# Kernel optimization log

Measured on AMD Instinct MI355X. Metric: run time of the kernel, lower is better.

The kernel has to match this reference:

```python
import jax, jax.numpy as jnp
import numpy as np

NQ = 14            # qubits = ceil(log2(16384))
DIM = 2 ** NQ
OUT = 1000         # out_features (slice last OUT probs)


def _apply_ry(state, theta, axis):
    """Apply RY(theta) on the qubit at `axis` of state shaped (B, 2,...,2).
    RY = [[cos(t/2), -sin(t/2)], [sin(t/2), cos(t/2)]] (real)."""
    c = jnp.cos(theta / 2)
    s = jnp.sin(theta / 2)
    x = jnp.moveaxis(state, axis, -1)
    x0, x1 = x[..., 0], x[..., 1]
    y = jnp.stack([c * x0 - s * x1, s * x0 + c * x1], axis=-1)
    return jnp.moveaxis(y, -1, axis)


def _apply_cz(state, axis):
    """CZ on adjacent qubits (axis, axis+1): flip sign of |11> amplitudes."""
    sign = jnp.ones((2, 2), state.dtype).at[1, 1].set(-1.0)
    shape = [1] * state.ndim
    shape[axis] = 2
    shape[axis + 1] = 2
    return state * sign.reshape(shape)


def _circuit(inp, weights, bias):
    B, F = inp.shape
    # AmplitudeEmbedding(pad_with=1, normalize=True)
    if F < DIM:
        inp = jnp.pad(inp, ((0, 0), (0, DIM - F)), constant_values=1.0)
    norm = jnp.sqrt(jnp.sum(inp * inp, axis=1, keepdims=True))
    state = (inp / norm).reshape((B,) + (2,) * NQ)
    # SimplifiedTwoDesign: initial RY layer (bias)
    for w in range(NQ):
        state = _apply_ry(state, bias[w], 1 + w)
    # entangling layers: even CZ/RY block then odd CZ/RY block
    nlayer = weights.shape[0]
    for l in range(nlayer):
        for start in (0, 1):
            for i in range(start, NQ - 1, 2):
                state = _apply_cz(state, 1 + i)
                state = _apply_ry(state, weights[l, i, 0], 1 + i)
                state = _apply_ry(state, weights[l, i, 1], 1 + i + 1)
    amps = state.reshape(B, DIM)
    probs = amps * amps  # real statevector -> |amp|^2
    return probs[:, -OUT:]


def setup_inputs() -> dict:
    key = jax.random.key(0)
    k1, k2, k3 = jax.random.split(key, 3)
    return {
        "input": jax.random.normal(k1, (512, 16384), dtype=jnp.float32),
        "weights": jax.random.normal(k2, (2, NQ - 1, 2), dtype=jnp.float32),
        "bias": jax.random.normal(k3, (NQ,), dtype=jnp.float32),
    }


def reference(input, weights, bias):
    return _circuit(input, weights, bias)
```

## Files before the change

### kernel.cpp

```cpp
#include <hip/hip_runtime.h>

#define NQ 14
#define DIM 16384
#define OUT_N 1000
#define PRUNED 2048

using v2f = __attribute__((ext_vector_type(2))) float;

__host__ __device__ constexpr int WI(int l, int i, int k) {
    return 14 + (l * 13 + i) * 2 + k;
}

__global__ void cs_kernel(const float* __restrict__ w,
                          const float* __restrict__ b,
                          float2* __restrict__ cs) {
    int g = threadIdx.x;
    if (g < 66) {
        float th = (g < NQ) ? b[g] : w[g - NQ];
        cs[g] = make_float2(cosf(0.5f * th), sinf(0.5f * th));
    }
}

__device__ __forceinline__ int swz(int a) { return a ^ ((a >> 5) & 31); }

template<int B, int NP>
__device__ __forceinline__ void ry(v2f* x, float c, float s) {
    if constexpr (B == 0) {
#pragma unroll
        for (int p = 0; p < NP; ++p) {
            float a0 = x[p].x, a1 = x[p].y;
            x[p].x = c * a0 - s * a1;
            x[p].y = s * a0 + c * a1;
        }
    } else {
        constexpr int pb = B - 1;
#pragma unroll
        for (int m = 0; m < NP / 2; ++m) {
            int p0 = ((m >> pb) << (pb + 1)) | (m & ((1 << pb) - 1));
            int p1 = p0 | (1 << pb);
            v2f lo = x[p0], hi = x[p1];
            x[p0] = lo * c - hi * s;
            x[p1] = hi * c + lo * s;
        }
    }
}

template<int BH, int BL, int NP>
__device__ __forceinline__ void cz(v2f* x) {
    static_assert(BH > BL, "");
    if constexpr (BL >= 1) {
#pragma unroll
        for (int p = 0; p < NP; ++p)
            if (((p >> (BH - 1)) & 1) && ((p >> (BL - 1)) & 1)) x[p] = -x[p];
    } else {
#pragma unroll
        for (int p = 0; p < NP; ++p)
            if ((p >> (BH - 1)) & 1) x[p].y = -x[p].y;
    }
}

#define BLK(BH, I0, I1, NP)                                       \
    cz<BH, BH - 1, NP>(x);                                        \
    { float2 cc = csv[I0]; ry<BH, NP>(x, cc.x, cc.y); }           \
    { float2 cd = csv[I1]; ry<BH - 1, NP>(x, cd.x, cd.y); }

__global__ __launch_bounds__(256, 2)
void qnnA(const float* __restrict__ in, const float2* __restrict__ csv,
          float* __restrict__ ws) {
    __shared__ float red[4];
    const int t = threadIdx.x;
    const int b = blockIdx.x;
    const float* __restrict__ xin = in + (size_t)b * DIM;

    v2f x[32];
#pragma unroll
    for (int p = 0; p < 32; ++p) {
        x[p].x = xin[((2 * p) << 8) | t];
        x[p].y = xin[((2 * p + 1) << 8) | t];
    }

    float pp = 0.f;
#pragma unroll
    for (int p = 0; p < 32; ++p) pp = fmaf(x[p].x, x[p].x, fmaf(x[p].y, x[p].y, pp));
#pragma unroll
    for (int d = 32; d; d >>= 1) pp += __shfl_xor(pp, d);
    if ((t & 63) == 0) red[t >> 6] = pp;
    __syncthreads();
    const float scale = 1.0f / sqrtf(red[0] + red[1] + red[2] + red[3]);

    { float2 cc;
      cc = csv[0]; ry<5, 32>(x, cc.x, cc.y);
      cc = csv[1]; ry<4, 32>(x, cc.x, cc.y);
      cc = csv[2]; ry<3, 32>(x, cc.x, cc.y);
      cc = csv[3]; ry<2, 32>(x, cc.x, cc.y);
      cc = csv[4]; ry<1, 32>(x, cc.x, cc.y);
      cc = csv[5]; ry<0, 32>(x, cc.x, cc.y); }
    BLK(5, WI(0,0,0), WI(0,0,1), 32)
    BLK(3, WI(0,2,0), WI(0,2,1), 32)
    BLK(1, WI(0,4,0), WI(0,4,1), 32)
    BLK(4, WI(0,1,0), WI(0,1,1), 32)
    BLK(2, WI(0,3,0), WI(0,3,1), 32)
    BLK(5, WI(1,0,0), WI(1,0,1), 32)
    BLK(3, WI(1,2,0), WI(1,2,1), 32)
    BLK(4, WI(1,1,0), WI(1,1,1), 32)

    float* __restrict__ wrow = ws + (size_t)b * PRUNED;
#pragma unroll
    for (int p = 28; p < 32; ++p) {
        wrow[((2 * p - 56) << 8) | t] = x[p].x * scale;
        wrow[((2 * p - 55) << 8) | t] = x[p].y * scale;
    }
}

__global__ __launch_bounds__(64, 4)
void qnnB(const float* __restrict__ ws, const float2* __restrict__ csv,
          float* __restrict__ out) {
    __shared__ float lds[PRUNED];
    const int s = threadIdx.x;
    const int r = blockIdx.x;

    v2f x[16];
    { const float4* __restrict__ src4 =
          (const float4*)(ws + (size_t)r * PRUNED + s * 32);
#pragma unroll
      for (int i = 0; i < 8; ++i) {
          float4 f = src4[i];
          x[2 * i].x = f.x; x[2 * i].y = f.y;
          x[2 * i + 1].x = f.z; x[2 * i + 1].y = f.w;
      } }

    { float2 cc;
      cc = csv[9];  ry<4, 16>(x, cc.x, cc.y);
      cc = csv[10]; ry<3, 16>(x, cc.x, cc.y);
      cc = csv[11]; ry<2, 16>(x, cc.x, cc.y);
      cc = csv[12]; ry<1, 16>(x, cc.x, cc.y);
      cc = csv[13]; ry<0, 16>(x, cc.x, cc.y); }
    BLK(3, WI(0,10,0), WI(0,10,1), 16)
    BLK(1, WI(0,12,0), WI(0,12,1), 16)
    BLK(2, WI(0,11,0), WI(0,11,1), 16)
    BLK(1, WI(1,12,0), WI(1,12,1), 16)

#pragma unroll
    for (int l = 0; l < 32; ++l)
        lds[swz((s << 5) | l)] = (l & 1) ? x[l >> 1].y : x[l >> 1].x;
    __syncthreads();
#pragma unroll
    for (int l = 0; l < 32; ++l) {
        float v = lds[swz(((s >> 4) << 9) | (l << 4) | (s & 15))];
        if (l & 1) x[l >> 1].y = v; else x[l >> 1].x = v;
    }

    { float2 cc;
      cc = csv[6]; ry<3, 16>(x, cc.x, cc.y);
      cc = csv[7]; ry<2, 16>(x, cc.x, cc.y);
      cc = csv[8]; ry<1, 16>(x, cc.x, cc.y); }
    BLK(3, WI(0,6,0), WI(0,6,1), 16)
    BLK(1, WI(0,8,0), WI(0,8,1), 16)
    BLK(4, WI(0,5,0), WI(0,5,1), 16)
    BLK(2, WI(0,7,0), WI(0,7,1), 16)
    BLK(3, WI(1,6,0), WI(1,6,1), 16)

#pragma unroll
    for (int l = 0; l < 32; ++l)
        lds[swz(((s >> 4) << 9) | (l << 4) | (s & 15))] =
            (l & 1) ? x[l >> 1].y : x[l >> 1].x;
    __syncthreads();
#pragma unroll
    for (int l = 0; l < 32; ++l) {
        float v = lds[swz(((s >> 2) << 7) | (l << 2) | (s & 3))];
        if (l & 1) x[l >> 1].y = v; else x[l >> 1].x = v;
    }

    BLK(2, WI(0,9,0),  WI(0,9,1),  16)
    BLK(3, WI(1,8,0),  WI(1,8,1),  16)
    BLK(1, WI(1,10,0), WI(1,10,1), 16)
    BLK(4, WI(1,7,0),  WI(1,7,1),  16)
    BLK(2, WI(1,9,0),  WI(1,9,1),  16)

#pragma unroll
    for (int l = 0; l < 32; ++l)
        lds[swz(((s >> 2) << 7) | (l << 2) | (s & 3))] =
            (l & 1) ? x[l >> 1].y : x[l >> 1].x;
    __syncthreads();
#pragma unroll
    for (int l = 0; l < 32; ++l) {
        float v = lds[swz((l << 6) | s)];
        if (l & 1) x[l >> 1].y = v; else x[l >> 1].x = v;
    }

    BLK(3, WI(1,4,0), WI(1,4,1), 16)
    BLK(4, WI(1,3,0), WI(1,3,1), 16)
    BLK(2, WI(1,5,0), WI(1,5,1), 16)

#pragma unroll
    for (int l = 0; l < 32; ++l)
        lds[swz((l << 6) | s)] = (l & 1) ? x[l >> 1].y : x[l >> 1].x;
    __syncthreads();
#pragma unroll
    for (int l = 0; l < 32; ++l) {
        float v = lds[swz((s << 5) | l)];
        if (l & 1) x[l >> 1].y = v; else x[l >> 1].x = v;
    }

    BLK(2, WI(1,11,0), WI(1,11,1), 16)

    if (s >= 32) {
        float* __restrict__ orow = out + (size_t)r * OUT_N;
        const int base = s * 32 - 1048;
#pragma unroll
        for (int l = 0; l < 32; ++l) {
            int j = base + l;
            float v = (l & 1) ? x[l >> 1].y : x[l >> 1].x;
            if (j >= 0) orow[j] = v * v;
        }
    }
}

extern "C" void kernel_launch(void* const* d_in, const int* in_sizes, int n_in,
                              void* d_out, int out_size, void* d_ws, size_t ws_size,
                              hipStream_t stream) {
    const float* in   = (const float*)d_in[0];
    const float* wts  = (const float*)d_in[1];
    const float* bias = (const float*)d_in[2];
    float* out = (float*)d_out;

    float2* cs  = (float2*)d_ws;
    float*  buf = (float*)d_ws + 1024;

    const int nb = in_sizes[0] / DIM;

    cs_kernel<<<1, 128, 0, stream>>>(wts, bias, cs);
    qnnA<<<nb, 256, 0, stream>>>(in, (const float2*)cs, buf);
    qnnB<<<nb, 64, 0, stream>>>(buf, (const float2*)cs, out);
}
```

Baseline: 92.06 us.

## Fuse three launches into one kernel with LDS transposes and vectorized loads

Merges the cos/sin precompute, stage A and stage B into a single kernel. Each block computes the gate coefficients into shared memory, loads its row with contiguous float4 reads, applies the high-qubit gates, transposes through a 64KB LDS buffer, then does the pruned tail on 64 threads through LDS instead of a global workspace round-trip. The aim is to remove launch overhead and the workspace write/read. The cost is 64KB of shared memory per block, which limits occupancy, and a serial tail where only one wavefront is active.

```diff
diff --git a/kernel.cpp b/kernel.cpp
--- a/kernel.cpp
+++ b/kernel.cpp
@@ -3,7 +3,6 @@
 #define NQ 14
 #define DIM 16384
 #define OUT_N 1000
-#define PRUNED 2048
 
 using v2f = __attribute__((ext_vector_type(2))) float;
 
@@ -11,17 +10,8 @@
     return 14 + (l * 13 + i) * 2 + k;
 }
 
-__global__ void cs_kernel(const float* __restrict__ w,
-                          const float* __restrict__ b,
-                          float2* __restrict__ cs) {
-    int g = threadIdx.x;
-    if (g < 66) {
-        float th = (g < NQ) ? b[g] : w[g - NQ];
-        cs[g] = make_float2(cosf(0.5f * th), sinf(0.5f * th));
-    }
-}
-
-__device__ __forceinline__ int swz(int a) { return a ^ ((a >> 5) & 31); }
+__device__ __forceinline__ int swzM(int e) { return e ^ ((e >> 6) & 31); }
+__device__ __forceinline__ int swzB(int a) { return a ^ ((a >> 5) & 31); }
 
 template<int B, int NP>
 __device__ __forceinline__ void ry(v2f* x, float c, float s) {
@@ -61,23 +51,32 @@
 
 #define BLK(BH, I0, I1, NP)                                       \
     cz<BH, BH - 1, NP>(x);                                        \
-    { float2 cc = csv[I0]; ry<BH, NP>(x, cc.x, cc.y); }           \
-    { float2 cd = csv[I1]; ry<BH - 1, NP>(x, cd.x, cd.y); }
+    { float2 cc = csl[I0]; ry<BH, NP>(x, cc.x, cc.y); }           \
+    { float2 cd = csl[I1]; ry<BH - 1, NP>(x, cd.x, cd.y); }
 
 __global__ __launch_bounds__(256, 2)
-void qnnA(const float* __restrict__ in, const float2* __restrict__ csv,
-          float* __restrict__ ws) {
+void qnn_fused(const float* __restrict__ in, const float* __restrict__ wts,
+               const float* __restrict__ bias, float* __restrict__ out) {
+    __shared__ float lds[DIM];
+    __shared__ float2 csl[66];
     __shared__ float red[4];
+
     const int t = threadIdx.x;
     const int b = blockIdx.x;
-    const float* __restrict__ xin = in + (size_t)b * DIM;
+
+    if (t < 66) {
+        float th = (t < NQ) ? bias[t] : wts[t - NQ];
+        csl[t] = make_float2(cosf(0.5f * th), sinf(0.5f * th));
+    }
 
     v2f x[32];
-#pragma unroll
-    for (int p = 0; p < 32; ++p) {
-        x[p].x = xin[((2 * p) << 8) | t];
-        x[p].y = xin[((2 * p + 1) << 8) | t];
-    }
+    { const float4* __restrict__ src4 = (const float4*)(in + (size_t)b * DIM + t * 64);
+#pragma unroll
+      for (int i = 0; i < 16; ++i) {
+          float4 f = src4[i];
+          x[2 * i].x = f.x;     x[2 * i].y = f.y;
+          x[2 * i + 1].x = f.z; x[2 * i + 1].y = f.w;
+      } }
 
     float pp = 0.f;
 #pragma unroll
@@ -89,12 +88,38 @@
     const float scale = 1.0f / sqrtf(red[0] + red[1] + red[2] + red[3]);
 
     { float2 cc;
-      cc = csv[0]; ry<5, 32>(x, cc.x, cc.y);
-      cc = csv[1]; ry<4, 32>(x, cc.x, cc.y);
-      cc = csv[2]; ry<3, 32>(x, cc.x, cc.y);
-      cc = csv[3]; ry<2, 32>(x, cc.x, cc.y);
-      cc = csv[4]; ry<1, 32>(x, cc.x, cc.y);
-      cc = csv[5]; ry<0, 32>(x, cc.x, cc.y); }
+      cc = csl[8];  ry<5, 32>(x, cc.x, cc.y);
+      cc = csl[9];  ry<4, 32>(x, cc.x, cc.y);
+      cc = csl[10]; ry<3, 32>(x, cc.x, cc.y);
+      cc = csl[11]; ry<2, 32>(x, cc.x, cc.y);
+      cc = csl[12]; ry<1, 32>(x, cc.x, cc.y);
+      cc = csl[13]; ry<0, 32>(x, cc.x, cc.y); }
+    BLK(5, WI(0,8,0),  WI(0,8,1),  32)
+    BLK(3, WI(0,10,0), WI(0,10,1), 32)
+    BLK(1, WI(0,12,0), WI(0,12,1), 32)
+    BLK(4, WI(0,9,0),  WI(0,9,1),  32)
+    BLK(2, WI(0,11,0), WI(0,11,1), 32)
+    BLK(3, WI(1,10,0), WI(1,10,1), 32)
+    BLK(1, WI(1,12,0), WI(1,12,1), 32)
+    BLK(2, WI(1,11,0), WI(1,11,1), 32)
+
+#pragma unroll
+    for (int r = 0; r < 64; ++r)
+        lds[swzM((t << 6) | r)] = (r & 1) ? x[r >> 1].y : x[r >> 1].x;
+    __syncthreads();
+#pragma unroll
+    for (int r = 0; r < 64; ++r) {
+        float v = lds[swzM((r << 8) | t)];
+        if (r & 1) x[r >> 1].y = v; else x[r >> 1].x = v;
+    }
+
+    { float2 cc;
+      cc = csl[0]; ry<5, 32>(x, cc.x, cc.y);
+      cc = csl[1]; ry<4, 32>(x, cc.x, cc.y);
+      cc = csl[2]; ry<3, 32>(x, cc.x, cc.y);
+      cc = csl[3]; ry<2, 32>(x, cc.x, cc.y);
+      cc = csl[4]; ry<1, 32>(x, cc.x, cc.y);
+      cc = csl[5]; ry<0, 32>(x, cc.x, cc.y); }
     BLK(5, WI(0,0,0), WI(0,0,1), 32)
     BLK(3, WI(0,2,0), WI(0,2,1), 32)
     BLK(1, WI(0,4,0), WI(0,4,1), 32)
@@ -104,114 +129,69 @@
     BLK(3, WI(1,2,0), WI(1,2,1), 32)
     BLK(4, WI(1,1,0), WI(1,1,1), 32)
 
-    float* __restrict__ wrow = ws + (size_t)b * PRUNED;
+    __syncthreads();
 #pragma unroll
     for (int p = 28; p < 32; ++p) {
-        wrow[((2 * p - 56) << 8) | t] = x[p].x * scale;
-        wrow[((2 * p - 55) << 8) | t] = x[p].y * scale;
-    }
-}
-
-__global__ __launch_bounds__(64, 4)
-void qnnB(const float* __restrict__ ws, const float2* __restrict__ csv,
-          float* __restrict__ out) {
-    __shared__ float lds[PRUNED];
-    const int s = threadIdx.x;
-    const int r = blockIdx.x;
-
-    v2f x[16];
-    { const float4* __restrict__ src4 =
-          (const float4*)(ws + (size_t)r * PRUNED + s * 32);
-#pragma unroll
-      for (int i = 0; i < 8; ++i) {
-          float4 f = src4[i];
-          x[2 * i].x = f.x; x[2 * i].y = f.y;
-          x[2 * i + 1].x = f.z; x[2 * i + 1].y = f.w;
-      } }
-
-    { float2 cc;
-      cc = csv[9];  ry<4, 16>(x, cc.x, cc.y);
-      cc = csv[10]; ry<3, 16>(x, cc.x, cc.y);
-      cc = csv[11]; ry<2, 16>(x, cc.x, cc.y);
-      cc = csv[12]; ry<1, 16>(x, cc.x, cc.y);
-      cc = csv[13]; ry<0, 16>(x, cc.x, cc.y); }
-    BLK(3, WI(0,10,0), WI(0,10,1), 16)
-    BLK(1, WI(0,12,0), WI(0,12,1), 16)
-    BLK(2, WI(0,11,0), WI(0,11,1), 16)
-    BLK(1, WI(1,12,0), WI(1,12,1), 16)
-
-#pragma unroll
-    for (int l = 0; l < 32; ++l)
-        lds[swz((s << 5) | l)] = (l & 1) ? x[l >> 1].y : x[l >> 1].x;
-    __syncthreads();
-#pragma unroll
-    for (int l = 0; l < 32; ++l) {
-        float v = lds[swz(((s >> 4) << 9) | (l << 4) | (s & 15))];
-        if (l & 1) x[l >> 1].y = v; else x[l >> 1].x = v;
-    }
-
-    { float2 cc;
-      cc = csv[6]; ry<3, 16>(x, cc.x, cc.y);
-      cc = csv[7]; ry<2, 16>(x, cc.x, cc.y);
-      cc = csv[8]; ry<1, 16>(x, cc.x, cc.y); }
-    BLK(3, WI(0,6,0), WI(0,6,1), 16)
-    BLK(1, WI(0,8,0), WI(0,8,1), 16)
-    BLK(4, WI(0,5,0), WI(0,5,1), 16)
-    BLK(2, WI(0,7,0), WI(0,7,1), 16)
-    BLK(3, WI(1,6,0), WI(1,6,1), 16)
-
-#pragma unroll
-    for (int l = 0; l < 32; ++l)
-        lds[swz(((s >> 4) << 9) | (l << 4) | (s & 15))] =
-            (l & 1) ? x[l >> 1].y : x[l >> 1].x;
-    __syncthreads();
-#pragma unroll
-    for (int l = 0; l < 32; ++l) {
-        float v = lds[swz(((s >> 2) << 7) | (l << 2) | (s & 3))];
-        if (l & 1) x[l >> 1].y = v; else x[l >> 1].x = v;
-    }
-
-    BLK(2, WI(0,9,0),  WI(0,9,1),  16)
-    BLK(3, WI(1,8,0),  WI(1,8,1),  16)
-    BLK(1, WI(1,10,0), WI(1,10,1), 16)
-    BLK(4, WI(1,7,0),  WI(1,7,1),  16)
-    BLK(2, WI(1,9,0),  WI(1,9,1),  16)
-
-#pragma unroll
-    for (int l = 0; l < 32; ++l)
-        lds[swz(((s >> 2) << 7) | (l << 2) | (s & 3))] =
-            (l & 1) ? x[l >> 1].y : x[l >> 1].x;
-    __syncthreads();
-#pragma unroll
-    for (int l = 0; l < 32; ++l) {
-        float v = lds[swz((l << 6) | s)];
-        if (l & 1) x[l >> 1].y = v; else x[l >> 1].x = v;
-    }
-
-    BLK(3, WI(1,4,0), WI(1,4,1), 16)
-    BLK(4, WI(1,3,0), WI(1,3,1), 16)
-    BLK(2, WI(1,5,0), WI(1,5,1), 16)
-
-#pragma unroll
-    for (int l = 0; l < 32; ++l)
-        lds[swz((l << 6) | s)] = (l & 1) ? x[l >> 1].y : x[l >> 1].x;
-    __syncthreads();
-#pragma unroll
-    for (int l = 0; l < 32; ++l) {
-        float v = lds[swz((s << 5) | l)];
-        if (l & 1) x[l >> 1].y = v; else x[l >> 1].x = v;
-    }
-
-    BLK(2, WI(1,11,0), WI(1,11,1), 16)
-
-    if (s >= 32) {
-        float* __restrict__ orow = out + (size_t)r * OUT_N;
-        const int base = s * 32 - 1048;
+        lds[swzB(((2 * p - 56) << 8) | t)] = x[p].x * scale;
+        lds[swzB(((2 * p - 55) << 8) | t)] = x[p].y * scale;
+    }
+    __syncthreads();
+
+    if (t < 64) {
+        const int s = t;
 #pragma unroll
         for (int l = 0; l < 32; ++l) {
-            int j = base + l;
-            float v = (l & 1) ? x[l >> 1].y : x[l >> 1].x;
-            if (j >= 0) orow[j] = v * v;
+            float v = lds[swzB((l << 6) | s)];
+            if (l & 1) x[l >> 1].y = v; else x[l >> 1].x = v;
+        }
+        { float2 cc;
+          cc = csl[6]; ry<1, 16>(x, cc.x, cc.y);
+          cc = csl[7]; ry<0, 16>(x, cc.x, cc.y); }
+        BLK(1, WI(0,6,0), WI(0,6,1), 16)
+        BLK(2, WI(0,5,0), WI(0,5,1), 16)
+        BLK(3, WI(1,4,0), WI(1,4,1), 16)
+        BLK(4, WI(1,3,0), WI(1,3,1), 16)
+#pragma unroll
+        for (int l = 0; l < 32; ++l)
+            lds[swzB((l << 6) | s)] = (l & 1) ? x[l >> 1].y : x[l >> 1].x;
+    }
+    __syncthreads();
+    if (t < 64) {
+        const int s = t;
+#pragma unroll
+        for (int l = 0; l < 32; ++l) {
+            float v = lds[swzB(((s >> 4) << 9) | (l << 4) | (s & 15))];
+            if (l & 1) x[l >> 1].y = v; else x[l >> 1].x = v;
+        }
+        BLK(2, WI(0,7,0), WI(0,7,1), 16)
+        BLK(3, WI(1,6,0), WI(1,6,1), 16)
+        BLK(1, WI(1,8,0), WI(1,8,1), 16)
+        BLK(4, WI(1,5,0), WI(1,5,1), 16)
+        BLK(2, WI(1,7,0), WI(1,7,1), 16)
+#pragma unroll
+        for (int l = 0; l < 32; ++l)
+            lds[swzB(((s >> 4) << 9) | (l << 4) | (s & 15))] =
+                (l & 1) ? x[l >> 1].y : x[l >> 1].x;
+    }
+    __syncthreads();
+    if (t < 64) {
+        const int s = t;
+#pragma unroll
+        for (int l = 0; l < 32; ++l) {
+            float v = lds[swzB(((s >> 2) << 7) | (l << 2) | (s & 3))];
+            if (l & 1) x[l >> 1].y = v; else x[l >> 1].x = v;
+        }
+        BLK(2, WI(1,9,0), WI(1,9,1), 16)
+
+        if (s >= 32) {
+            float* __restrict__ orow = out + (size_t)b * OUT_N;
+            const int base = ((s >> 2) << 7) | (s & 3);
+#pragma unroll
+            for (int l = 0; l < 32; ++l) {
+                int j = base + (l << 2) - 1048;
+                float v = (l & 1) ? x[l >> 1].y : x[l >> 1].x;
+                if (j >= 0) orow[j] = v * v;
+            }
         }
     }
 }
@@ -224,12 +204,6 @@
     const float* bias = (const float*)d_in[2];
     float* out = (float*)d_out;
 
-    float2* cs  = (float2*)d_ws;
-    float*  buf = (float*)d_ws + 1024;
-
     const int nb = in_sizes[0] / DIM;
-
-    cs_kernel<<<1, 128, 0, stream>>>(wts, bias, cs);
-    qnnA<<<nb, 256, 0, stream>>>(in, (const float2*)cs, buf);
-    qnnB<<<nb, 64, 0, stream>>>(buf, (const float2*)cs, out);
-}
+    qnn_fused<<<nb, 256, 0, stream>>>(in, wts, bias, out);
+}
```

Measured after the change: 96.89 us. 5.2% more time.
